# Kernel optimization log

Hardware: AMD Instinct MI355X
Metric: run time of the kernel (lower is better)

The kernel has to match this reference:

```python
import jax, jax.numpy as jnp
import numpy as np

B, N, FIN, FOUT, H = 8, 2048, 128, 128, 2


def setup_inputs() -> dict:
    key = jax.random.key(0)
    k_h, k_adj, k_w, k_a = jax.random.split(key, 4)
    h = jax.random.normal(k_h, (B, N, FIN), dtype=jnp.float32)
    adj = jax.random.randint(k_adj, (B, N, N), 0, 2).astype(jnp.int32)
    # self-loops so no softmax row is all -inf
    idx = jnp.arange(N)
    adj = adj.at[:, idx, idx].set(1)
    W = jax.random.normal(k_w, (H, FIN, FOUT), dtype=jnp.float32) * 0.1
    a = jax.random.normal(k_a, (H, 2 * FOUT), dtype=jnp.float32) * 0.1
    return {"h": h, "adj": adj, "W": W, "a": a}


def reference(h, adj, W, a):
    # h: [B,N,FIN], adj: [B,N,N] int, W: [H,FIN,FOUT], a: [H,2*FOUT]
    Fout = W.shape[-1]
    Wh = jnp.einsum('bnf,hfo->bhno', h, W)              # [B,H,N,FOUT]
    # decompose a^T [Wh_i || Wh_j] = a1.Wh_i + a2.Wh_j (exact same math,
    # avoids the [B,N,N,2F] concat the torch code materializes)
    a1, a2 = a[:, :Fout], a[:, Fout:]
    s_i = jnp.einsum('bhno,ho->bhn', Wh, a1)            # score from node i
    s_j = jnp.einsum('bhno,ho->bhn', Wh, a2)            # score from node j
    e = jax.nn.leaky_relu(s_i[:, :, :, None] + s_j[:, :, None, :], 0.2)  # [B,H,N,N]
    e = jnp.where(adj[:, None, :, :] == 0, -jnp.inf, e)
    att = jax.nn.softmax(e, axis=-1)                    # [B,H,N,N]
    out = jnp.einsum('bhnm,bhmo->bhno', att, Wh)        # [B,H,N,FOUT]
    b, hh, n, f = out.shape
    # concat heads along feature dim (head order matches torch cat)
    return out.transpose(0, 2, 1, 3).reshape(b, n, hh * f)
```

## Files before the change

### kernel.cpp

```cpp
#include <hip/hip_runtime.h>
#include <math.h>

constexpr int Bv   = 8;
constexpr int Nv   = 2048;
constexpr int FIN  = 128;
constexpr int FOUT = 128;
constexpr int NH   = 2;
constexpr float LOG2E = 1.44269504088896340736f;

typedef __attribute__((ext_vector_type(8))) short  short8;
typedef __attribute__((ext_vector_type(4))) float  f32x4;
typedef __attribute__((ext_vector_type(4))) int    i32x4;

static __device__ __forceinline__ unsigned short f2bf(float f) {
    unsigned u = __builtin_bit_cast(unsigned, f);
    u += 0x7fffu + ((u >> 16) & 1u);
    return (unsigned short)(u >> 16);
}
static __device__ __forceinline__ float bf2f(unsigned short s) {
    unsigned u = ((unsigned)s) << 16;
    return __builtin_bit_cast(float, u);
}
static __device__ __forceinline__ float fast_exp2(float x) {
#if __has_builtin(__builtin_amdgcn_exp2f)
    return __builtin_amdgcn_exp2f(x);
#else
    return exp2f(x);
#endif
}
static __device__ __forceinline__ unsigned cvt_pk_bf16(float lo, float hi) {
    unsigned r;
    asm("v_cvt_pk_bf16_f32 %0, %1, %2" : "=v"(r) : "v"(lo), "v"(hi));
    return r;
}

__global__ void wa_kernel(const float* __restrict__ W, const float* __restrict__ a,
                          float* __restrict__ wa) {
    int hh = blockIdx.x;
    int t = threadIdx.x;
    int f = t >> 1, half = t & 1;
    const float* Wr = W + ((size_t)hh * FIN + f) * FOUT + half * 64;
    const float* ar = a + (size_t)hh * 2 * FOUT + half * 64;
    float s1 = 0.f, s2 = 0.f;
    for (int o = 0; o < 64; o += 4) {
        float4 w4 = *(const float4*)&Wr[o];
        s1 += w4.x * ar[o] + w4.y * ar[o + 1] + w4.z * ar[o + 2] + w4.w * ar[o + 3];
        s2 += w4.x * ar[FOUT + o] + w4.y * ar[FOUT + o + 1] + w4.z * ar[FOUT + o + 2] + w4.w * ar[FOUT + o + 3];
    }
    s1 += __shfl_xor(s1, 1, 64);
    s2 += __shfl_xor(s2, 1, 64);
    if (half == 0) {
        wa[(hh * 2 + 0) * FIN + f] = s1 * LOG2E;
        wa[(hh * 2 + 1) * FIN + f] = s2 * LOG2E;
    }
}

__global__ __launch_bounds__(256) void sij_kernel(const float* __restrict__ h,
                                                  const float* __restrict__ wa,
                                                  float* __restrict__ si,
                                                  float* __restrict__ sj) {
    int row  = blockIdx.x * 4 + (threadIdx.x >> 6);
    int lane = threadIdx.x & 63;
    float x0 = h[(size_t)row * FIN + lane];
    float x1 = h[(size_t)row * FIN + 64 + lane];
    float s[4];
#pragma unroll
    for (int q = 0; q < 4; ++q) {
        const float* w = wa + q * FIN;
        s[q] = x0 * w[lane] + x1 * w[64 + lane];
    }
#pragma unroll
    for (int m = 32; m >= 1; m >>= 1) {
#pragma unroll
        for (int q = 0; q < 4; ++q) s[q] += __shfl_xor(s[q], m, 64);
    }
    if (lane == 0) {
        int bb = row >> 11, n = row & (Nv - 1);
        si[((size_t)(bb * NH + 0)) * Nv + n] = s[0];
        sj[((size_t)(bb * NH + 0)) * Nv + n] = s[1];
        si[((size_t)(bb * NH + 1)) * Nv + n] = s[2];
        sj[((size_t)(bb * NH + 1)) * Nv + n] = s[3];
    }
}

__global__ __launch_bounds__(256) void pack_kernel(const int* __restrict__ adj,
                                                   unsigned long long* __restrict__ adjp) {
    int wid = blockIdx.x * 4 + (threadIdx.x >> 6);
    int l   = threadIdx.x & 63;
    int b   = wid >> 11;
    int r5  = wid & 2047;
    int jt  = r5 >> 6;
    int rb  = r5 & 63;
    const int* src = adj + ((size_t)b * Nv + rb * 32) * Nv + jt * 64 + l;
    unsigned long long* dst = adjp + ((size_t)b * 32 + jt) * Nv + rb * 32;
    for (int r = 0; r < 32; r += 4) {
        int a0 = src[(size_t)(r + 0) * Nv];
        int a1 = src[(size_t)(r + 1) * Nv];
        int a2 = src[(size_t)(r + 2) * Nv];
        int a3 = src[(size_t)(r + 3) * Nv];
        unsigned long long b0 = __ballot(a0 != 0);
        unsigned long long b1 = __ballot(a1 != 0);
        unsigned long long b2 = __ballot(a2 != 0);
        unsigned long long b3 = __ballot(a3 != 0);
        if (l == 0) {
            uint4 q0 = {(unsigned)b0, (unsigned)(b0 >> 32), (unsigned)b1, (unsigned)(b1 >> 32)};
            uint4 q1 = {(unsigned)b2, (unsigned)(b2 >> 32), (unsigned)b3, (unsigned)(b3 >> 32)};
            *(uint4*)&dst[r]     = q0;
            *(uint4*)&dst[r + 2] = q1;
        }
    }
}

__global__ __launch_bounds__(256, 2) void wh_kernel(const float* __restrict__ h,
                                                    const float* __restrict__ W,
                                                    unsigned short* __restrict__ whf) {
    int bid = blockIdx.x;
    int bb  = bid & 7;
    int r   = bid >> 3;
    int hh  = r & 1;
    int n0  = (r >> 1) * 64;
    int jtb = n0 >> 6;

    __shared__ unsigned short Whi[FIN * 132];
    __shared__ unsigned short Wlo[FIN * 132];

    int t = threadIdx.x;
    const float* Ws = W + (size_t)hh * FIN * FOUT;
    for (int idx = t; idx < FIN * FOUT; idx += 256) {
        int f = idx >> 7, o = idx & 127;
        float wv = Ws[idx];
        unsigned short uh = f2bf(wv);
        Whi[o * 132 + f] = uh;
        Wlo[o * 132 + f] = f2bf(wv - bf2f(uh));
    }
    __syncthreads();

    int w = t >> 6, l = t & 63, lo16 = l & 15, grp = l >> 4;
    int o0 = w * 32;

    short8 ahi[2][4], alo[2][4];
#pragma unroll
    for (int ot = 0; ot < 2; ++ot)
#pragma unroll
        for (int kt = 0; kt < 4; ++kt) {
            int off = (o0 + ot * 16 + lo16) * 132 + kt * 32 + grp * 8;
            ahi[ot][kt] = *(const short8*)&Whi[off];
            alo[ot][kt] = *(const short8*)&Wlo[off];
        }

    f32x4 acc[2][4];
#pragma unroll
    for (int ot = 0; ot < 2; ++ot)
#pragma unroll
        for (int nt = 0; nt < 4; ++nt) acc[ot][nt] = (f32x4){0.f, 0.f, 0.f, 0.f};

    const float* hb = h + ((size_t)bb * Nv + n0) * FIN;
#pragma unroll
    for (int nt = 0; nt < 4; ++nt) {
#pragma unroll
        for (int kt = 0; kt < 4; ++kt) {
            const float* hp = hb + (size_t)(nt * 16 + lo16) * FIN + kt * 32 + grp * 8;
            float4 x0 = *(const float4*)hp;
            float4 x1 = *(const float4*)(hp + 4);
            float xs[8] = {x0.x, x0.y, x0.z, x0.w, x1.x, x1.y, x1.z, x1.w};
            short8 bhi, blo;
#pragma unroll
            for (int i = 0; i < 8; ++i) {
                unsigned short uh = f2bf(xs[i]);
                bhi[i] = (short)uh;
                blo[i] = (short)f2bf(xs[i] - bf2f(uh));
            }
#pragma unroll
            for (int ot = 0; ot < 2; ++ot) {
                acc[ot][nt] = __builtin_amdgcn_mfma_f32_16x16x32_bf16(ahi[ot][kt], bhi, acc[ot][nt], 0, 0, 0);
                acc[ot][nt] = __builtin_amdgcn_mfma_f32_16x16x32_bf16(ahi[ot][kt], blo, acc[ot][nt], 0, 0, 0);
                acc[ot][nt] = __builtin_amdgcn_mfma_f32_16x16x32_bf16(alo[ot][kt], bhi, acc[ot][nt], 0, 0, 0);
            }
        }
    }
    unsigned short* db = whf + (size_t)(bb * NH + hh) * 32 * 8192;
#pragma unroll
    for (int ot = 0; ot < 2; ++ot)
#pragma unroll
        for (int nt = 0; nt < 4; ++nt)
#pragma unroll
            for (int reg = 0; reg < 4; ++reg) {
                int o  = o0 + ot * 16 + grp * 4 + reg;
                int n  = nt * 16 + lo16;
                int kt = n >> 5, gf = (n >> 3) & 3, i = n & 7;
                int ct = o >> 4, lf = o & 15;
                db[((((size_t)jtb * 8 + ct) * 2 + kt) * 64 + gf * 16 + lf) * 8 + i] =
                    f2bf(acc[ot][nt][reg]);
            }
}

__global__ __launch_bounds__(256, 4) void gat_attn_kernel(
    const unsigned long long* __restrict__ adjp, const unsigned short* __restrict__ whf,
    const float* __restrict__ si, const float* __restrict__ sj,
    float* __restrict__ out) {
    int bid   = blockIdx.x;
    int bb    = bid & 7;
    int r2    = bid >> 3;
    int itile = r2 & 63;
    int ch    = r2 >> 6;

    int t = threadIdx.x;
    int w = t >> 6, l = t & 63, lo16 = l & 15, grp = l >> 4;
    int h = w >> 1, rh = w & 1;
    int r0 = itile * 32 + rh * 16;
    int myrow = r0 + lo16;

    float sir = si[(size_t)(bb * NH + h) * Nv + myrow];
    const unsigned long long* adjr = adjp + (size_t)bb * 32 * Nv + myrow;
    const float*          sjb = sj + (size_t)(bb * NH + h) * Nv;
    const unsigned short* wb  = whf + (size_t)(bb * NH + h) * 32 * 8192 + ch * 4096;

    f32x4 acc[4], accL;
#pragma unroll
    for (int ct = 0; ct < 4; ++ct) acc[ct] = (f32x4){0.f, 0.f, 0.f, 0.f};
    accL = (f32x4){0.f, 0.f, 0.f, 0.f};

    const int ones_w = 0x3f803f80;
    short8 onesf = __builtin_bit_cast(short8, (i32x4){ones_w, ones_w, ones_w, ones_w});

    unsigned long long m0, m1;
    float4 sv0[2][2], sv1[2][2];

    auto ldmeta = [&](unsigned long long& m, float4 (&sv)[2][2], int jt) {
        m = adjr[(size_t)jt * Nv];
        int jb = jt * 64;
#pragma unroll
        for (int kt = 0; kt < 2; ++kt) {
            sv[kt][0] = *(const float4*)&sjb[jb + kt * 32 + grp * 8];
            sv[kt][1] = *(const float4*)&sjb[jb + kt * 32 + grp * 8 + 4];
        }
    };
    ldmeta(m0, sv0, 0);

    auto body = [&](unsigned long long& mc, float4 (&svc)[2][2],
                    unsigned long long& mn, float4 (&svn)[2][2], int jt) {
        const unsigned short* jbp = wb + (size_t)jt * 8192 + (size_t)l * 8;
        short8 bf[4][2];
#pragma unroll
        for (int ct = 0; ct < 4; ++ct) {
            bf[ct][0] = *(const short8*)(jbp + (ct * 2 + 0) * 512);
            bf[ct][1] = *(const short8*)(jbp + (ct * 2 + 1) * 512);
        }
        if (jt < 31) ldmeta(mn, svn, jt + 1);

        unsigned mw0 = (unsigned)mc, mw1 = (unsigned)(mc >> 32);
        short8 af[2];
#pragma unroll
        for (int kt = 0; kt < 2; ++kt) {
            unsigned mb = ((kt ? mw1 : mw0) >> (grp * 8)) & 0xFFu;
            unsigned ws[4];
#pragma unroll
            for (int hf = 0; hf < 2; ++hf) {
                float4 s4 = svc[kt][hf];
                float x0 = sir + s4.x, x1 = sir + s4.y, x2 = sir + s4.z, x3 = sir + s4.w;
                x0 = fmaxf(x0, 0.2f * x0); x1 = fmaxf(x1, 0.2f * x1);
                x2 = fmaxf(x2, 0.2f * x2); x3 = fmaxf(x3, 0.2f * x3);
                float p0 = fast_exp2(x0), p1 = fast_exp2(x1);
                float p2 = fast_exp2(x2), p3 = fast_exp2(x3);
                p0 = (mb & (1u << (hf * 4 + 0))) ? p0 : 0.f;
                p1 = (mb & (1u << (hf * 4 + 1))) ? p1 : 0.f;
                p2 = (mb & (1u << (hf * 4 + 2))) ? p2 : 0.f;
                p3 = (mb & (1u << (hf * 4 + 3))) ? p3 : 0.f;
                ws[hf * 2 + 0] = cvt_pk_bf16(p0, p1);
                ws[hf * 2 + 1] = cvt_pk_bf16(p2, p3);
            }
            af[kt] = __builtin_bit_cast(short8, (i32x4){(int)ws[0], (int)ws[1], (int)ws[2], (int)ws[3]});
        }
#pragma unroll
        for (int ct = 0; ct < 4; ++ct) {
            acc[ct] = __builtin_amdgcn_mfma_f32_16x16x32_bf16(af[0], bf[ct][0], acc[ct], 0, 0, 0);
            acc[ct] = __builtin_amdgcn_mfma_f32_16x16x32_bf16(af[1], bf[ct][1], acc[ct], 0, 0, 0);
        }
        accL = __builtin_amdgcn_mfma_f32_16x16x32_bf16(af[0], onesf, accL, 0, 0, 0);
        accL = __builtin_amdgcn_mfma_f32_16x16x32_bf16(af[1], onesf, accL, 0, 0, 0);
    };

    for (int jt = 0; jt < 32; jt += 2) {
        body(m0, sv0, m1, sv1, jt);
        body(m1, sv1, m0, sv0, jt + 1);
    }

#pragma unroll
    for (int reg = 0; reg < 4; ++reg) {
        float linv = 1.0f / accL[reg];
        int   row  = r0 + grp * 4 + reg;
        float* op = out + ((size_t)(bb * Nv + row)) * (NH * FOUT) + h * FOUT + ch * 64;
#pragma unroll
        for (int ct = 0; ct < 4; ++ct)
            op[ct * 16 + lo16] = acc[ct][reg] * linv;
    }
}

extern "C" void kernel_launch(void* const* d_in, const int* in_sizes, int n_in,
                              void* d_out, int out_size, void* d_ws, size_t ws_size,
                              hipStream_t stream) {
    const float* h   = (const float*)d_in[0];
    const int*   adj = (const int*)d_in[1];
    const float* W   = (const float*)d_in[2];
    const float* a   = (const float*)d_in[3];
    float*       out = (float*)d_out;

    char* ws = (char*)d_ws;
    unsigned short*     whf  = (unsigned short*)ws;
    unsigned long long* adjp = (unsigned long long*)(ws + 8388608);
    float* si = (float*)(ws + 8388608 + 4194304);
    float* sj = si + (size_t)Bv * NH * Nv;
    float* wa = sj + (size_t)Bv * NH * Nv;

    wa_kernel  <<<dim3(2),                  dim3(256), 0, stream>>>(W, a, wa);
    sij_kernel <<<dim3(Bv * Nv / 4),        dim3(256), 0, stream>>>(h, wa, si, sj);
    pack_kernel<<<dim3(4096),               dim3(256), 0, stream>>>(adj, adjp);
    wh_kernel  <<<dim3(Bv * NH * (Nv/64)),  dim3(256), 0, stream>>>(h, W, whf);
    gat_attn_kernel<<<dim3(Bv * (Nv/32) * 2), dim3(256), 0, stream>>>(adjp, whf, si, sj, out);
}
```

Measured before the change: 113.6 us.

## Merge prep kernels and switch attention to 32x32 MFMA with split-K reduction

The adjacency pack, score, and Wh projection kernels are merged into one prep launch that dispatches on block index, which removes launch overhead and lets the stages overlap. The attention kernel now uses 32x32x16 bf16 MFMA tiles over 64-row blocks. The key range is split across wave pairs and their partial results are combined through shared memory. The Wh fragment layout is changed to match the new MFMA operand order. The trade-offs are more accumulator registers (occupancy hint lowered from 4 to 3), a shared-memory reduction with a barrier, and fewer blocks in the attention grid.

```diff
diff --git a/kernel.cpp b/kernel.cpp
--- a/kernel.cpp
+++ b/kernel.cpp
@@ -8,9 +8,11 @@
 constexpr int NH   = 2;
 constexpr float LOG2E = 1.44269504088896340736f;
 
-typedef __attribute__((ext_vector_type(8))) short  short8;
-typedef __attribute__((ext_vector_type(4))) float  f32x4;
-typedef __attribute__((ext_vector_type(4))) int    i32x4;
+typedef __attribute__((ext_vector_type(8)))  short short8;
+typedef __attribute__((ext_vector_type(4)))  float f32x4;
+typedef __attribute__((ext_vector_type(16))) float f32x16;
+typedef __attribute__((ext_vector_type(4)))  int   i32x4;
+typedef unsigned long long u64;
 
 static __device__ __forceinline__ unsigned short f2bf(float f) {
     unsigned u = __builtin_bit_cast(unsigned, f);
@@ -55,244 +57,240 @@
     }
 }
 
-__global__ __launch_bounds__(256) void sij_kernel(const float* __restrict__ h,
-                                                  const float* __restrict__ wa,
-                                                  float* __restrict__ si,
-                                                  float* __restrict__ sj) {
-    int row  = blockIdx.x * 4 + (threadIdx.x >> 6);
-    int lane = threadIdx.x & 63;
-    float x0 = h[(size_t)row * FIN + lane];
-    float x1 = h[(size_t)row * FIN + 64 + lane];
-    float s[4];
-#pragma unroll
-    for (int q = 0; q < 4; ++q) {
-        const float* w = wa + q * FIN;
-        s[q] = x0 * w[lane] + x1 * w[64 + lane];
-    }
-#pragma unroll
-    for (int m = 32; m >= 1; m >>= 1) {
-#pragma unroll
-        for (int q = 0; q < 4; ++q) s[q] += __shfl_xor(s[q], m, 64);
-    }
-    if (lane == 0) {
-        int bb = row >> 11, n = row & (Nv - 1);
-        si[((size_t)(bb * NH + 0)) * Nv + n] = s[0];
-        sj[((size_t)(bb * NH + 0)) * Nv + n] = s[1];
-        si[((size_t)(bb * NH + 1)) * Nv + n] = s[2];
-        sj[((size_t)(bb * NH + 1)) * Nv + n] = s[3];
-    }
-}
-
-__global__ __launch_bounds__(256) void pack_kernel(const int* __restrict__ adj,
-                                                   unsigned long long* __restrict__ adjp) {
-    int wid = blockIdx.x * 4 + (threadIdx.x >> 6);
-    int l   = threadIdx.x & 63;
-    int b   = wid >> 11;
-    int r5  = wid & 2047;
-    int jt  = r5 >> 6;
-    int rb  = r5 & 63;
-    const int* src = adj + ((size_t)b * Nv + rb * 32) * Nv + jt * 64 + l;
-    unsigned long long* dst = adjp + ((size_t)b * 32 + jt) * Nv + rb * 32;
-    for (int r = 0; r < 32; r += 4) {
-        int a0 = src[(size_t)(r + 0) * Nv];
-        int a1 = src[(size_t)(r + 1) * Nv];
-        int a2 = src[(size_t)(r + 2) * Nv];
-        int a3 = src[(size_t)(r + 3) * Nv];
-        unsigned long long b0 = __ballot(a0 != 0);
-        unsigned long long b1 = __ballot(a1 != 0);
-        unsigned long long b2 = __ballot(a2 != 0);
-        unsigned long long b3 = __ballot(a3 != 0);
-        if (l == 0) {
-            uint4 q0 = {(unsigned)b0, (unsigned)(b0 >> 32), (unsigned)b1, (unsigned)(b1 >> 32)};
-            uint4 q1 = {(unsigned)b2, (unsigned)(b2 >> 32), (unsigned)b3, (unsigned)(b3 >> 32)};
-            *(uint4*)&dst[r]     = q0;
-            *(uint4*)&dst[r + 2] = q1;
-        }
-    }
-}
-
-__global__ __launch_bounds__(256, 2) void wh_kernel(const float* __restrict__ h,
-                                                    const float* __restrict__ W,
-                                                    unsigned short* __restrict__ whf) {
+__global__ __launch_bounds__(256, 2) void prep_kernel(
+    const float* __restrict__ h, const float* __restrict__ W,
+    const int* __restrict__ adj, const float* __restrict__ wa,
+    u64* __restrict__ adjp, unsigned short* __restrict__ whf,
+    float* __restrict__ si, float* __restrict__ sj) {
+    __shared__ unsigned short Whi[FIN * 132];
+    __shared__ unsigned short Wlo[FIN * 132];
+
+    int bid = blockIdx.x;
+    int t   = threadIdx.x;
+
+    if (bid < 4096) {
+        int wid = bid * 4 + (t >> 6);
+        int l   = t & 63;
+        int b   = wid >> 11;
+        int r5  = wid & 2047;
+        int jt  = r5 >> 6;
+        int rb  = r5 & 63;
+        const int* src = adj + ((size_t)b * Nv + rb * 32) * Nv + jt * 64 + l;
+        u64* dst = adjp + ((size_t)b * 32 + jt) * Nv + rb * 32;
+        for (int r = 0; r < 32; r += 8) {
+            int av[8];
+#pragma unroll
+            for (int k = 0; k < 8; ++k) av[k] = src[(size_t)(r + k) * Nv];
+            u64 m[8];
+#pragma unroll
+            for (int k = 0; k < 8; ++k) m[k] = __ballot(av[k] != 0);
+            if (l == 0) {
+#pragma unroll
+                for (int k = 0; k < 8; k += 2) {
+                    uint4 q = {(unsigned)m[k], (unsigned)(m[k] >> 32),
+                               (unsigned)m[k + 1], (unsigned)(m[k + 1] >> 32)};
+                    *(uint4*)&dst[r + k] = q;
+                }
+            }
+        }
+    } else if (bid < 8192) {
+        int row  = (bid - 4096) * 4 + (t >> 6);
+        int lane = t & 63;
+        float x0 = h[(size_t)row * FIN + lane];
+        float x1 = h[(size_t)row * FIN + 64 + lane];
+        float s[4];
+#pragma unroll
+        for (int q = 0; q < 4; ++q) {
+            const float* wp = wa + q * FIN;
+            s[q] = x0 * wp[lane] + x1 * wp[64 + lane];
+        }
+#pragma unroll
+        for (int m = 32; m >= 1; m >>= 1) {
+#pragma unroll
+            for (int q = 0; q < 4; ++q) s[q] += __shfl_xor(s[q], m, 64);
+        }
+        if (lane == 0) {
+            int bb = row >> 11, n = row & (Nv - 1);
+            si[((size_t)(bb * NH + 0)) * Nv + n] = s[0];
+            sj[((size_t)(bb * NH + 0)) * Nv + n] = s[1];
+            si[((size_t)(bb * NH + 1)) * Nv + n] = s[2];
+            sj[((size_t)(bb * NH + 1)) * Nv + n] = s[3];
+        }
+    } else {
+        int wb2 = bid - 8192;
+        int bb  = wb2 & 7;
+        int r2  = wb2 >> 3;
+        int hh  = r2 & 1;
+        int jtb = r2 >> 1;
+        int n0  = jtb * 64;
+
+        const float* Ws = W + (size_t)hh * FIN * FOUT;
+        for (int idx = t; idx < FIN * FOUT; idx += 256) {
+            int f = idx >> 7, o = idx & 127;
+            float wv = Ws[idx];
+            unsigned short uh = f2bf(wv);
+            Whi[o * 132 + f] = uh;
+            Wlo[o * 132 + f] = f2bf(wv - bf2f(uh));
+        }
+        __syncthreads();
+
+        int w = t >> 6, l = t & 63, lo16 = l & 15, grp = l >> 4;
+        int o0 = w * 32;
+
+        short8 ahi[2][4], alo[2][4];
+#pragma unroll
+        for (int ot = 0; ot < 2; ++ot)
+#pragma unroll
+            for (int kt = 0; kt < 4; ++kt) {
+                int off = (o0 + ot * 16 + lo16) * 132 + kt * 32 + grp * 8;
+                ahi[ot][kt] = *(const short8*)&Whi[off];
+                alo[ot][kt] = *(const short8*)&Wlo[off];
+            }
+
+        f32x4 acc[2][4];
+#pragma unroll
+        for (int ot = 0; ot < 2; ++ot)
+#pragma unroll
+            for (int nt = 0; nt < 4; ++nt) acc[ot][nt] = (f32x4){0.f, 0.f, 0.f, 0.f};
+
+        const float* hb = h + ((size_t)bb * Nv + n0) * FIN;
+#pragma unroll
+        for (int nt = 0; nt < 4; ++nt) {
+#pragma unroll
+            for (int kt = 0; kt < 4; ++kt) {
+                const float* hp = hb + (size_t)(nt * 16 + lo16) * FIN + kt * 32 + grp * 8;
+                float4 x0 = *(const float4*)hp;
+                float4 x1 = *(const float4*)(hp + 4);
+                float xs[8] = {x0.x, x0.y, x0.z, x0.w, x1.x, x1.y, x1.z, x1.w};
+                short8 bhi, blo;
+#pragma unroll
+                for (int i = 0; i < 8; ++i) {
+                    unsigned short uh = f2bf(xs[i]);
+                    bhi[i] = (short)uh;
+                    blo[i] = (short)f2bf(xs[i] - bf2f(uh));
+                }
+#pragma unroll
+                for (int ot = 0; ot < 2; ++ot) {
+                    acc[ot][nt] = __builtin_amdgcn_mfma_f32_16x16x32_bf16(ahi[ot][kt], bhi, acc[ot][nt], 0, 0, 0);
+                    acc[ot][nt] = __builtin_amdgcn_mfma_f32_16x16x32_bf16(ahi[ot][kt], blo, acc[ot][nt], 0, 0, 0);
+                    acc[ot][nt] = __builtin_amdgcn_mfma_f32_16x16x32_bf16(alo[ot][kt], bhi, acc[ot][nt], 0, 0, 0);
+                }
+            }
+        }
+        unsigned short* db = whf + (size_t)(bb * NH + hh) * 262144;
+#pragma unroll
+        for (int ot = 0; ot < 2; ++ot)
+#pragma unroll
+            for (int nt = 0; nt < 4; ++nt)
+#pragma unroll
+                for (int reg = 0; reg < 4; ++reg) {
+                    int oc = ot * 16 + grp * 4 + reg;
+                    db[(size_t)(((jtb * 4 + nt) * 4 + w) * 64 + (lo16 >> 3) * 32 + oc) * 8 + (lo16 & 7)] =
+                        f2bf(acc[ot][nt][reg]);
+                }
+    }
+}
+
+__global__ __launch_bounds__(256, 3) void gat_attn_kernel(
+    const u64* __restrict__ adjp, const unsigned short* __restrict__ whf,
+    const float* __restrict__ si, const float* __restrict__ sj,
+    float* __restrict__ out) {
     int bid = blockIdx.x;
     int bb  = bid & 7;
-    int r   = bid >> 3;
-    int hh  = r & 1;
-    int n0  = (r >> 1) * 64;
-    int jtb = n0 >> 6;
-
-    __shared__ unsigned short Whi[FIN * 132];
-    __shared__ unsigned short Wlo[FIN * 132];
-
-    int t = threadIdx.x;
-    const float* Ws = W + (size_t)hh * FIN * FOUT;
-    for (int idx = t; idx < FIN * FOUT; idx += 256) {
-        int f = idx >> 7, o = idx & 127;
-        float wv = Ws[idx];
-        unsigned short uh = f2bf(wv);
-        Whi[o * 132 + f] = uh;
-        Wlo[o * 132 + f] = f2bf(wv - bf2f(uh));
-    }
-    __syncthreads();
-
-    int w = t >> 6, l = t & 63, lo16 = l & 15, grp = l >> 4;
-    int o0 = w * 32;
-
-    short8 ahi[2][4], alo[2][4];
-#pragma unroll
-    for (int ot = 0; ot < 2; ++ot)
-#pragma unroll
-        for (int kt = 0; kt < 4; ++kt) {
-            int off = (o0 + ot * 16 + lo16) * 132 + kt * 32 + grp * 8;
-            ahi[ot][kt] = *(const short8*)&Whi[off];
-            alo[ot][kt] = *(const short8*)&Wlo[off];
-        }
-
-    f32x4 acc[2][4];
-#pragma unroll
-    for (int ot = 0; ot < 2; ++ot)
-#pragma unroll
-        for (int nt = 0; nt < 4; ++nt) acc[ot][nt] = (f32x4){0.f, 0.f, 0.f, 0.f};
-
-    const float* hb = h + ((size_t)bb * Nv + n0) * FIN;
-#pragma unroll
-    for (int nt = 0; nt < 4; ++nt) {
-#pragma unroll
-        for (int kt = 0; kt < 4; ++kt) {
-            const float* hp = hb + (size_t)(nt * 16 + lo16) * FIN + kt * 32 + grp * 8;
-            float4 x0 = *(const float4*)hp;
-            float4 x1 = *(const float4*)(hp + 4);
-            float xs[8] = {x0.x, x0.y, x0.z, x0.w, x1.x, x1.y, x1.z, x1.w};
-            short8 bhi, blo;
-#pragma unroll
-            for (int i = 0; i < 8; ++i) {
-                unsigned short uh = f2bf(xs[i]);
-                bhi[i] = (short)uh;
-                blo[i] = (short)f2bf(xs[i] - bf2f(uh));
-            }
-#pragma unroll
-            for (int ot = 0; ot < 2; ++ot) {
-                acc[ot][nt] = __builtin_amdgcn_mfma_f32_16x16x32_bf16(ahi[ot][kt], bhi, acc[ot][nt], 0, 0, 0);
-                acc[ot][nt] = __builtin_amdgcn_mfma_f32_16x16x32_bf16(ahi[ot][kt], blo, acc[ot][nt], 0, 0, 0);
-                acc[ot][nt] = __builtin_amdgcn_mfma_f32_16x16x32_bf16(alo[ot][kt], bhi, acc[ot][nt], 0, 0, 0);
-            }
-        }
-    }
-    unsigned short* db = whf + (size_t)(bb * NH + hh) * 32 * 8192;
-#pragma unroll
-    for (int ot = 0; ot < 2; ++ot)
-#pragma unroll
-        for (int nt = 0; nt < 4; ++nt)
-#pragma unroll
-            for (int reg = 0; reg < 4; ++reg) {
-                int o  = o0 + ot * 16 + grp * 4 + reg;
-                int n  = nt * 16 + lo16;
-                int kt = n >> 5, gf = (n >> 3) & 3, i = n & 7;
-                int ct = o >> 4, lf = o & 15;
-                db[((((size_t)jtb * 8 + ct) * 2 + kt) * 64 + gf * 16 + lf) * 8 + i] =
-                    f2bf(acc[ot][nt][reg]);
-            }
-}
-
-__global__ __launch_bounds__(256, 4) void gat_attn_kernel(
-    const unsigned long long* __restrict__ adjp, const unsigned short* __restrict__ whf,
-    const float* __restrict__ si, const float* __restrict__ sj,
-    float* __restrict__ out) {
-    int bid   = blockIdx.x;
-    int bb    = bid & 7;
-    int r2    = bid >> 3;
-    int itile = r2 & 63;
-    int ch    = r2 >> 6;
-
-    int t = threadIdx.x;
-    int w = t >> 6, l = t & 63, lo16 = l & 15, grp = l >> 4;
-    int h = w >> 1, rh = w & 1;
-    int r0 = itile * 32 + rh * 16;
-    int myrow = r0 + lo16;
-
-    float sir = si[(size_t)(bb * NH + h) * Nv + myrow];
-    const unsigned long long* adjr = adjp + (size_t)bb * 32 * Nv + myrow;
-    const float*          sjb = sj + (size_t)(bb * NH + h) * Nv;
-    const unsigned short* wb  = whf + (size_t)(bb * NH + h) * 32 * 8192 + ch * 4096;
-
-    f32x4 acc[4], accL;
-#pragma unroll
-    for (int ct = 0; ct < 4; ++ct) acc[ct] = (f32x4){0.f, 0.f, 0.f, 0.f};
-    accL = (f32x4){0.f, 0.f, 0.f, 0.f};
+    int r2  = bid >> 3;
+    int rp  = r2 & 31;
+    int hh  = (r2 >> 5) & 1;
+    int ch  = r2 >> 6;
+
+    int t = threadIdx.x, w = t >> 6, l = t & 63;
+    int jp = w & 1, rw = w >> 1;
+    int lo32 = l & 31, kh = l >> 5;
+    int r0 = rp * 64 + rw * 32;
+    int myrow = r0 + lo32;
+
+    float sir = si[(size_t)(bb * NH + hh) * Nv + myrow];
+    const u64*   adjr = adjp + (size_t)bb * 32 * Nv + myrow;
+    const float* sjb  = sj + (size_t)(bb * NH + hh) * Nv;
+    const unsigned short* wbp = whf + (size_t)(bb * NH + hh) * 262144 + (size_t)l * 8;
+
+    f32x16 acc0, acc1, accL;
+#pragma unroll
+    for (int i = 0; i < 16; ++i) { acc0[i] = 0.f; acc1[i] = 0.f; accL[i] = 0.f; }
 
     const int ones_w = 0x3f803f80;
     short8 onesf = __builtin_bit_cast(short8, (i32x4){ones_w, ones_w, ones_w, ones_w});
 
-    unsigned long long m0, m1;
-    float4 sv0[2][2], sv1[2][2];
-
-    auto ldmeta = [&](unsigned long long& m, float4 (&sv)[2][2], int jt) {
-        m = adjr[(size_t)jt * Nv];
+    int jt0 = jp * 16;
+    u64 mask = adjr[(size_t)jt0 * Nv];
+    for (int jtl = 0; jtl < 16; ++jtl) {
+        int jt = jt0 + jtl;
         int jb = jt * 64;
-#pragma unroll
-        for (int kt = 0; kt < 2; ++kt) {
-            sv[kt][0] = *(const float4*)&sjb[jb + kt * 32 + grp * 8];
-            sv[kt][1] = *(const float4*)&sjb[jb + kt * 32 + grp * 8 + 4];
-        }
-    };
-    ldmeta(m0, sv0, 0);
-
-    auto body = [&](unsigned long long& mc, float4 (&svc)[2][2],
-                    unsigned long long& mn, float4 (&svn)[2][2], int jt) {
-        const unsigned short* jbp = wb + (size_t)jt * 8192 + (size_t)l * 8;
+        const unsigned short* fb = wbp + (size_t)(jt * 16 + ch * 2) * 512;
         short8 bf[4][2];
 #pragma unroll
-        for (int ct = 0; ct < 4; ++ct) {
-            bf[ct][0] = *(const short8*)(jbp + (ct * 2 + 0) * 512);
-            bf[ct][1] = *(const short8*)(jbp + (ct * 2 + 1) * 512);
-        }
-        if (jt < 31) ldmeta(mn, svn, jt + 1);
-
-        unsigned mw0 = (unsigned)mc, mw1 = (unsigned)(mc >> 32);
-        short8 af[2];
-#pragma unroll
-        for (int kt = 0; kt < 2; ++kt) {
-            unsigned mb = ((kt ? mw1 : mw0) >> (grp * 8)) & 0xFFu;
-            unsigned ws[4];
-#pragma unroll
-            for (int hf = 0; hf < 2; ++hf) {
-                float4 s4 = svc[kt][hf];
-                float x0 = sir + s4.x, x1 = sir + s4.y, x2 = sir + s4.z, x3 = sir + s4.w;
-                x0 = fmaxf(x0, 0.2f * x0); x1 = fmaxf(x1, 0.2f * x1);
-                x2 = fmaxf(x2, 0.2f * x2); x3 = fmaxf(x3, 0.2f * x3);
-                float p0 = fast_exp2(x0), p1 = fast_exp2(x1);
-                float p2 = fast_exp2(x2), p3 = fast_exp2(x3);
-                p0 = (mb & (1u << (hf * 4 + 0))) ? p0 : 0.f;
-                p1 = (mb & (1u << (hf * 4 + 1))) ? p1 : 0.f;
-                p2 = (mb & (1u << (hf * 4 + 2))) ? p2 : 0.f;
-                p3 = (mb & (1u << (hf * 4 + 3))) ? p3 : 0.f;
-                ws[hf * 2 + 0] = cvt_pk_bf16(p0, p1);
-                ws[hf * 2 + 1] = cvt_pk_bf16(p2, p3);
-            }
-            af[kt] = __builtin_bit_cast(short8, (i32x4){(int)ws[0], (int)ws[1], (int)ws[2], (int)ws[3]});
-        }
-#pragma unroll
-        for (int ct = 0; ct < 4; ++ct) {
-            acc[ct] = __builtin_amdgcn_mfma_f32_16x16x32_bf16(af[0], bf[ct][0], acc[ct], 0, 0, 0);
-            acc[ct] = __builtin_amdgcn_mfma_f32_16x16x32_bf16(af[1], bf[ct][1], acc[ct], 0, 0, 0);
-        }
-        accL = __builtin_amdgcn_mfma_f32_16x16x32_bf16(af[0], onesf, accL, 0, 0, 0);
-        accL = __builtin_amdgcn_mfma_f32_16x16x32_bf16(af[1], onesf, accL, 0, 0, 0);
-    };
-
-    for (int jt = 0; jt < 32; jt += 2) {
-        body(m0, sv0, m1, sv1, jt);
-        body(m1, sv1, m0, sv0, jt + 1);
-    }
-
-#pragma unroll
-    for (int reg = 0; reg < 4; ++reg) {
-        float linv = 1.0f / accL[reg];
-        int   row  = r0 + grp * 4 + reg;
-        float* op = out + ((size_t)(bb * Nv + row)) * (NH * FOUT) + h * FOUT + ch * 64;
-#pragma unroll
-        for (int ct = 0; ct < 4; ++ct)
-            op[ct * 16 + lo16] = acc[ct][reg] * linv;
+        for (int kt = 0; kt < 4; ++kt) {
+            bf[kt][0] = *(const short8*)(fb + (kt * 4 + 0) * 512);
+            bf[kt][1] = *(const short8*)(fb + (kt * 4 + 1) * 512);
+        }
+        u64 mcur = mask;
+        if (jtl < 15) mask = adjr[(size_t)(jt + 1) * Nv];
+
+        short8 af[4];
+#pragma unroll
+        for (int kt = 0; kt < 4; ++kt) {
+            unsigned mb = (unsigned)(mcur >> (kt * 16 + kh * 8)) & 0xFFu;
+            const float* sp = &sjb[jb + kt * 16 + kh * 8];
+            float4 s0 = *(const float4*)sp;
+            float4 s1 = *(const float4*)(sp + 4);
+            float x0 = sir + s0.x, x1 = sir + s0.y, x2 = sir + s0.z, x3 = sir + s0.w;
+            float x4 = sir + s1.x, x5 = sir + s1.y, x6 = sir + s1.z, x7 = sir + s1.w;
+            x0 = fmaxf(x0, 0.2f * x0); x1 = fmaxf(x1, 0.2f * x1);
+            x2 = fmaxf(x2, 0.2f * x2); x3 = fmaxf(x3, 0.2f * x3);
+            x4 = fmaxf(x4, 0.2f * x4); x5 = fmaxf(x5, 0.2f * x5);
+            x6 = fmaxf(x6, 0.2f * x6); x7 = fmaxf(x7, 0.2f * x7);
+            float p0 = fast_exp2(x0), p1 = fast_exp2(x1), p2 = fast_exp2(x2), p3 = fast_exp2(x3);
+            float p4 = fast_exp2(x4), p5 = fast_exp2(x5), p6 = fast_exp2(x6), p7 = fast_exp2(x7);
+            p0 = (mb & 1u)   ? p0 : 0.f;  p1 = (mb & 2u)   ? p1 : 0.f;
+            p2 = (mb & 4u)   ? p2 : 0.f;  p3 = (mb & 8u)   ? p3 : 0.f;
+            p4 = (mb & 16u)  ? p4 : 0.f;  p5 = (mb & 32u)  ? p5 : 0.f;
+            p6 = (mb & 64u)  ? p6 : 0.f;  p7 = (mb & 128u) ? p7 : 0.f;
+            unsigned w0 = cvt_pk_bf16(p0, p1), w1 = cvt_pk_bf16(p2, p3);
+            unsigned w2 = cvt_pk_bf16(p4, p5), w3 = cvt_pk_bf16(p6, p7);
+            af[kt] = __builtin_bit_cast(short8, (i32x4){(int)w0, (int)w1, (int)w2, (int)w3});
+        }
+#pragma unroll
+        for (int kt = 0; kt < 4; ++kt) {
+            acc0 = __builtin_amdgcn_mfma_f32_32x32x16_bf16(af[kt], bf[kt][0], acc0, 0, 0, 0);
+            acc1 = __builtin_amdgcn_mfma_f32_32x32x16_bf16(af[kt], bf[kt][1], acc1, 0, 0, 0);
+            accL = __builtin_amdgcn_mfma_f32_32x32x16_bf16(af[kt], onesf,    accL, 0, 0, 0);
+        }
+    }
+
+    __shared__ float red[2][64][49];
+    if (jp == 1) {
+#pragma unroll
+        for (int i = 0; i < 16; ++i) {
+            red[rw][l][i]      = acc0[i];
+            red[rw][l][16 + i] = acc1[i];
+            red[rw][l][32 + i] = accL[i];
+        }
+    }
+    __syncthreads();
+    if (jp == 0) {
+#pragma unroll
+        for (int i = 0; i < 16; ++i) {
+            acc0[i] += red[rw][l][i];
+            acc1[i] += red[rw][l][16 + i];
+            accL[i] += red[rw][l][32 + i];
+        }
+#pragma unroll
+        for (int reg = 0; reg < 16; ++reg) {
+            int rowc = (reg & 3) + 8 * (reg >> 2) + 4 * kh;
+            float linv = 1.0f / accL[reg];
+            float* op = out + ((size_t)(bb * Nv + r0 + rowc)) * (NH * FOUT) + hh * FOUT + ch * 64;
+            op[lo32]      = acc0[reg] * linv;
+            op[32 + lo32] = acc1[reg] * linv;
+        }
     }
 }
 
@@ -306,15 +304,13 @@
     float*       out = (float*)d_out;
 
     char* ws = (char*)d_ws;
-    unsigned short*     whf  = (unsigned short*)ws;
-    unsigned long long* adjp = (unsigned long long*)(ws + 8388608);
+    unsigned short* whf  = (unsigned short*)ws;
+    u64*            adjp = (u64*)(ws + 8388608);
     float* si = (float*)(ws + 8388608 + 4194304);
     float* sj = si + (size_t)Bv * NH * Nv;
     float* wa = sj + (size_t)Bv * NH * Nv;
 
-    wa_kernel  <<<dim3(2),                  dim3(256), 0, stream>>>(W, a, wa);
-    sij_kernel <<<dim3(Bv * Nv / 4),        dim3(256), 0, stream>>>(h, wa, si, sj);
-    pack_kernel<<<dim3(4096),               dim3(256), 0, stream>>>(adj, adjp);
-    wh_kernel  <<<dim3(Bv * NH * (Nv/64)),  dim3(256), 0, stream>>>(h, W, whf);
-    gat_attn_kernel<<<dim3(Bv * (Nv/32) * 2), dim3(256), 0, stream>>>(adjp, whf, si, sj, out);
-}
+    wa_kernel  <<<dim3(2),    dim3(256), 0, stream>>>(W, a, wa);
+    prep_kernel<<<dim3(8704), dim3(256), 0, stream>>>(h, W, adj, wa, adjp, whf, si, sj);
+    gat_attn_kernel<<<dim3(1024), dim3(256), 0, stream>>>(adjp, whf, si, sj, out);
+}
```

New measurement: 105.2 us. 7.5% less time.
